# Kernel optimization log

Hardware: AMD Instinct MI355X
Metric: run time of the kernel (lower is better)

Reference implementation:

```python
import jax, jax.numpy as jnp
import numpy as np
from jax.scipy.special import i0

# torchkbnufft default configuration
N = 256          # image size per dim (im_size)
OSF = 2          # grid oversampling factor (default grid_size = 2*im_size)
G = N * OSF      # oversampled grid size = 512
W = 6            # kernel width (numpoints default)
ALPHA = 2.34 * W # Kaiser-Bessel shape parameter (kbwidth default 2.34)
M = 65536        # number of non-uniform k-space samples
B, C = 2, 8      # batch, coils


def _kb_ft(t):
    """Analytic Fourier transform of the KB kernel (for deapodization)."""
    s2 = ALPHA ** 2 - (jnp.pi * W * t) ** 2
    z = jnp.sqrt(jnp.abs(s2)) + 1e-12
    return jnp.where(s2 >= 0, jnp.sinh(z) / z, jnp.sin(z) / z)


def _kb(d):
    """Kaiser-Bessel interpolation kernel, d = distance in grid units."""
    u = 1.0 - (2.0 * d / W) ** 2
    return jnp.where(u > 0, i0(ALPHA * jnp.sqrt(jnp.maximum(u, 1e-12))), 0.0) / W


def setup_inputs() -> dict:
    key = jax.random.key(0)
    k1, k2 = jax.random.split(key)
    x_image = jax.random.normal(k1, (B, C, N, N), dtype=jnp.float32)
    # trajectory in radians/sample, uniform in [-pi, pi)
    k_traj = (jax.random.uniform(k2, (2, M), dtype=jnp.float32) - 0.5) * (2 * jnp.pi)
    return {"x_image": x_image, "k_traj": k_traj}


def reference(x_image, k_traj):
    # 1) deapodization (scaling coefficients), centered image convention
    n = jnp.arange(N, dtype=jnp.float32) - N / 2
    sc = 1.0 / _kb_ft(n / G)                       # (N,)
    xs = (x_image * (sc[:, None] * sc[None, :])).astype(jnp.complex64)

    # 2) zero-pad onto oversampled grid with image centered at index 0 (mod G)
    grid = jnp.zeros(x_image.shape[:2] + (G, G), jnp.complex64)
    grid = grid.at[..., :N, :N].set(xs)
    grid = jnp.roll(grid, shift=(-(N // 2), -(N // 2)), axis=(-2, -1))
    Xk = jnp.fft.fft2(grid)                        # (B,C,G,G) uniform k-space

    # 3) KB interpolation onto non-uniform points (irregular gather)
    tm = k_traj * (G / (2 * jnp.pi))               # continuous grid coords, (2,M)
    offs = jnp.arange(-(W // 2) + 1, W // 2 + 1, dtype=jnp.float32)  # [-2..3]
    base = jnp.floor(tm)
    pts = base[:, :, None] + offs                  # (2,M,W) neighbor coords
    wts = _kb(tm[:, :, None] - pts)                # (2,M,W) real weights
    idx = pts.astype(jnp.int32) % G                # wrap (periodic grid)

    gathered = Xk[:, :, idx[0][:, :, None], idx[1][:, None, :]]  # (B,C,M,W,W)
    y = jnp.einsum('bcmij,mi,mj->bcm', gathered,
                   wts[0].astype(jnp.complex64), wts[1].astype(jnp.complex64))
    # return complex result as stacked (real, imag) float32 for the harness
    return jnp.stack([y.real, y.imag], axis=-1)   # (B,C,M,2)
```

## Files before the change

kernel.cpp:

```cpp
#include <hip/hip_runtime.h>
#include <hip/hip_fp16.h>
#include <math.h>

#define NN 256
#define GSZ 512
#define GG (GSZ * GSZ)
#define BC 16
#define MM 65536
#define ALPHA_C 14.04f
#define WKER 6
#define PI_F 3.14159265358979f
#define RC2 0.70710678118654752f
#define KSCALE 81.48733086305042f

#define SSCALE 16777216.0f
#define INV_SSCALE 5.9604644775390625e-8f

#define CAP 144
#define TRW 21
#define TPITCH 23
#define PLANE (TRW * TPITCH)
#define QPL 4
#define NPQ (QPL * TRW * TRW)

__device__ __forceinline__ __half2* gh_plane(float2* grid, int bc) {
    return (__half2*)((char*)grid + (size_t)bc * (GG * 8) + 524288);
}
__device__ __forceinline__ const __half2* gh_plane_c(const float2* grid, int bc) {
    return (const __half2*)((const char*)grid + (size_t)bc * (GG * 8) + 524288);
}


__device__ __forceinline__ float bessel_i0(float x) {
    if (x < 3.75f) {
        float t = x * (1.0f / 3.75f);
        float t2 = t * t;
        return 1.0f + t2 * (3.5156229f + t2 * (3.0899424f + t2 * (1.2067492f +
                     t2 * (0.2659732f + t2 * (0.0360768f + t2 * 0.0045813f)))));
    } else {
        float t = 3.75f / x;
        float p = 0.39894228f + t * (0.01328592f + t * (0.00225319f + t * (-0.00157565f +
                  t * (0.00916281f + t * (-0.02057706f + t * (0.02635537f +
                  t * (-0.01647633f + t * 0.00392377f)))))));
        return p * __expf(x) * rsqrtf(x);
    }
}

__device__ __forceinline__ float kb_weight(float d) {
    float r = d * (2.0f / (float)WKER);
    float u = 1.0f - r * r;
    if (u <= 0.0f) return 0.0f;
    return bessel_i0(ALPHA_C * sqrtf(u)) * (1.0f / (float)WKER);
}

__device__ __forceinline__ float kb_ft_inv(float t) {
    float a = PI_F * (float)WKER * t;
    float s2 = ALPHA_C * ALPHA_C - a * a;
    float z = sqrtf(fabsf(s2)) + 1e-12f;
    float sh = 0.5f * (__expf(z) - __expf(-z));
    return z / sh;
}

__device__ __forceinline__ void cmul(float& zr, float& zi, float wr, float wi) {
    float r = zr * wr - zi * wi;
    zi = zr * wi + zi * wr;
    zr = r;
}


template <int L>
__device__ __forceinline__ void radix8_stage(float* pr, float* pi_, int j) {
    int pos = j & (L - 1);
    int base = (j - pos) * 8 + pos;
    float ar[8], ai[8];
#pragma unroll
    for (int r = 0; r < 8; ++r) {
        int idx = base + r * L;
        int ph = idx + (idx >> 3);
        ar[r] = pr[ph];
        ai[r] = pi_[ph];
    }
    if (L > 1) {
        float th = (float)pos * (-PI_F / (4.0f * (float)L));
        float s1, c1;
        __sincosf(th, &s1, &c1);
        float wr = c1, wi = s1;
#pragma unroll
        for (int r = 1; r < 8; ++r) {
            cmul(ar[r], ai[r], wr, wi);
            float nr = wr * c1 - wi * s1;
            wi = wr * s1 + wi * c1;
            wr = nr;
        }
    }
    float s0r = ar[0] + ar[4], s0i = ai[0] + ai[4];
    float d0r = ar[0] - ar[4], d0i = ai[0] - ai[4];
    float s1r = ar[2] + ar[6], s1i = ai[2] + ai[6];
    float d1r = ar[2] - ar[6], d1i = ai[2] - ai[6];
    float E0r = s0r + s1r, E0i = s0i + s1i;
    float E2r = s0r - s1r, E2i = s0i - s1i;
    float E1r = d0r + d1i, E1i = d0i - d1r;
    float E3r = d0r - d1i, E3i = d0i + d1r;
    float u0r = ar[1] + ar[5], u0i = ai[1] + ai[5];
    float v0r = ar[1] - ar[5], v0i = ai[1] - ai[5];
    float u1r = ar[3] + ar[7], u1i = ai[3] + ai[7];
    float v1r = ar[3] - ar[7], v1i = ai[3] - ai[7];
    float O0r = u0r + u1r, O0i = u0i + u1i;
    float O2r = u0r - u1r, O2i = u0i - u1i;
    float O1r = v0r + v1i, O1i = v0i - v1r;
    float O3r = v0r - v1i, O3i = v0i + v1r;
    float t1r = RC2 * (O1r + O1i), t1i = RC2 * (O1i - O1r);
    float t2r = O2i,               t2i = -O2r;
    float t3r = RC2 * (O3i - O3r), t3i = -RC2 * (O3r + O3i);
    float xr[8], xi[8];
    xr[0] = E0r + O0r; xi[0] = E0i + O0i;
    xr[4] = E0r - O0r; xi[4] = E0i - O0i;
    xr[1] = E1r + t1r; xi[1] = E1i + t1i;
    xr[5] = E1r - t1r; xi[5] = E1i - t1i;
    xr[2] = E2r + t2r; xi[2] = E2i + t2i;
    xr[6] = E2r - t2r; xi[6] = E2i - t2i;
    xr[3] = E3r + t3r; xi[3] = E3i + t3i;
    xr[7] = E3r - t3r; xi[7] = E3i - t3i;
#pragma unroll
    for (int q = 0; q < 8; ++q) {
        int idx = base + q * L;
        int ph = idx + (idx >> 3);
        pr[ph] = xr[q];
        pi_[ph] = xi[q];
    }
}


#define LDSP 576
#define ROWBLK (BC * 64)
__global__ void __launch_bounds__(256) k_fft_row_bin(
    const float* __restrict__ x, float2* __restrict__ grid,
    const float* __restrict__ kt, unsigned* __restrict__ cnt,
    unsigned* __restrict__ meta, __half2* __restrict__ whalf) {
    __shared__ float re[4][LDSP], im[4][LDSP];
    int b = blockIdx.x;
    int t = threadIdx.x;
    if (b >= ROWBLK) {
        int m = (b - ROWBLK) * 256 + t;
        float tmx = kt[m] * KSCALE;
        float tmy = kt[MM + m] * KSCALE;
        float bx = floorf(tmx), by = floorf(tmy);
        int ibx = (int)bx & (GSZ - 1);
        int iby = (int)by & (GSZ - 1);
        int tile = ((ibx >> 4) << 5) | (iby >> 4);
        unsigned slot = atomicAdd(&cnt[tile], 1u);
        if (slot < CAP) {
            int idx = tile * CAP + (int)slot;
            int lx = ibx & 15;
            int ly = iby & 15;
            meta[idx] = ((unsigned)m << 8) | (unsigned)(lx << 4) | (unsigned)ly;
            float w0[6], w1[6];
#pragma unroll
            for (int o = 0; o < 6; ++o) {
                float offv = (float)(o - 2);
                w0[o] = kb_weight(tmx - (bx + offv));
                w1[o] = kb_weight(tmy - (by + offv));
            }
            __half2* wp = whalf + (size_t)idx * 6;
            wp[0] = __half2(__float2half_rn(w0[0]), __float2half_rn(w0[1]));
            wp[1] = __half2(__float2half_rn(w0[2]), __float2half_rn(w0[3]));
            wp[2] = __half2(__float2half_rn(w0[4]), __float2half_rn(w0[5]));
            wp[3] = __half2(__float2half_rn(w1[0]), __float2half_rn(w1[1]));
            wp[4] = __half2(__float2half_rn(w1[2]), __float2half_rn(w1[3]));
            wp[5] = __half2(__float2half_rn(w1[4]), __float2half_rn(w1[5]));
        }
        return;
    }
    int w = t >> 6;
    int l = t & 63;
    int rg = (b & 63) * 4 + w;
    int bc = b >> 6;
    int r = (rg < 128) ? rg : rg + 256;
    int r_img = rg ^ 128;
    float scx = kb_ft_inv((float)(r_img - 128) * (1.0f / (float)GSZ));
    const float* xrow = x + ((size_t)bc * NN + (size_t)r_img) * NN;
#pragma unroll
    for (int e = 0; e < 8; ++e) {
        int i = e * 64 + l;
        float v = 0.0f;
        if (i < 128 || i >= 384) {
            int y = (i + 128) & (GSZ - 1);
            float scy = kb_ft_inv((float)(y - 128) * (1.0f / (float)GSZ));
            v = xrow[y] * scx * scy;
        }
        int rev = (l & 7) * 64 + (l >> 3) * 8 + e;
        int ph = rev + (rev >> 3);
        re[w][ph] = v;
        im[w][ph] = 0.0f;
    }
    __syncthreads();
    radix8_stage<1>(re[w], im[w], l);
    __syncthreads();
    radix8_stage<8>(re[w], im[w], l);
    __syncthreads();
    radix8_stage<64>(re[w], im[w], l);
    __syncthreads();
    size_t gbase = (size_t)bc * GG + (size_t)r * GSZ;
#pragma unroll
    for (int e = 0; e < 8; ++e) {
        int k = e * 64 + l;
        int ph = k + (k >> 3);
        grid[gbase + k] = make_float2(re[w][ph], im[w][ph]);
    }
}


#define CSTR 577
__global__ void __launch_bounds__(256) k_fft_col(float2* __restrict__ grid) {
    __shared__ float re[16][CSTR], im[16][CSTR];
    int b = blockIdx.x;
    int bc = b >> 5;
    int c0 = (b & 31) << 4;
    size_t base = (size_t)bc * GG + (size_t)c0;
    int t = threadIdx.x;
#pragma unroll
    for (int it = 0; it < 32; ++it) {
        int idx = it * 256 + t;
        int row = idx >> 4, col = idx & 15;
        float2 v = make_float2(0.0f, 0.0f);
        if (row < 128 || row >= 384)
            v = grid[base + (size_t)row * GSZ + col];
        int rev = (row & 7) * 64 + ((row >> 3) & 7) * 8 + (row >> 6);
        int ph = rev + (rev >> 3);
        re[col][ph] = v.x;
        im[col][ph] = v.y;
    }
    __syncthreads();
    int col = t & 15, jg = t >> 4;
#pragma unroll
    for (int k = 0; k < 4; ++k) radix8_stage<1>(re[col], im[col], jg + 16 * k);
    __syncthreads();
#pragma unroll
    for (int k = 0; k < 4; ++k) radix8_stage<8>(re[col], im[col], jg + 16 * k);
    __syncthreads();
#pragma unroll
    for (int k = 0; k < 4; ++k) radix8_stage<64>(re[col], im[col], jg + 16 * k);
    __syncthreads();
    __half2* ghp = gh_plane(grid, bc);
#pragma unroll
    for (int it = 0; it < 32; ++it) {
        int idx = it * 256 + t;
        int row = idx >> 4, c = idx & 15;
        int ph = row + (row >> 3);
        ghp[(size_t)row * GSZ + c0 + c] = __float22half2_rn(
            make_float2(re[c][ph] * SSCALE, im[c][ph] * SSCALE));
    }
}


__global__ void __launch_bounds__(128, 6) k_gather_tile(
    const float2* __restrict__ grid, const unsigned* __restrict__ cnt,
    const unsigned* __restrict__ meta, const __half2* __restrict__ whalf,
    float2* __restrict__ out) {
    __shared__ __half2 ldsh[QPL * PLANE];
    int bid = blockIdx.x;
    int b = ((bid & 7) << 9) | (bid >> 3);
    int tile = b >> 2;
    int quad = b & 3;
    int bc0 = quad * QPL;
    int tx0 = (tile >> 5) << 4;
    int ty0 = (tile & 31) << 4;
    int t = threadIdx.x;
#pragma unroll
    for (int k = 0; k < 14; ++k) {
        int idx = t + (k << 7);
        if (idx < NPQ) {
            int p = idx / (TRW * TRW);
            int rem = idx - p * (TRW * TRW);
            int r = rem / TRW;
            int c = rem - r * TRW;
            int row = (tx0 - 2 + r) & (GSZ - 1);
            int col = (ty0 - 2 + c) & (GSZ - 1);
            ldsh[p * PLANE + r * TPITCH + c] =
                gh_plane_c(grid, bc0 + p)[(size_t)row * GSZ + col];
        }
    }
    int n = (int)cnt[tile];
    if (n > CAP) n = CAP;
    __syncthreads();
    int g = t >> 6;
    int baseA = (2 * g) * PLANE;
    int baseB = baseA + PLANE;
    int bcA = bc0 + 2 * g, bcB = bcA + 1;
    for (int s = (t & 63); s < n; s += 64) {
        int idx = tile * CAP + s;
        unsigned mc = meta[idx];
        int m = (int)(mc >> 8);
        int lx = (int)((mc >> 4) & 15u);
        int ly = (int)(mc & 15u);
        const __half2* wp = whalf + (size_t)idx * 6;
        __half2 p0 = wp[0], p1 = wp[1], p2 = wp[2];
        __half2 q0 = wp[3], q1 = wp[4], q2 = wp[5];
        float w0v[6], w1v[6];
        w0v[0] = __low2float(p0) * INV_SSCALE;
        w0v[1] = __high2float(p0) * INV_SSCALE;
        w0v[2] = __low2float(p1) * INV_SSCALE;
        w0v[3] = __high2float(p1) * INV_SSCALE;
        w0v[4] = __low2float(p2) * INV_SSCALE;
        w0v[5] = __high2float(p2) * INV_SSCALE;
        w1v[0] = __low2float(q0);
        w1v[1] = __high2float(q0);
        w1v[2] = __low2float(q1);
        w1v[3] = __high2float(q1);
        w1v[4] = __low2float(q2);
        w1v[5] = __high2float(q2);
        int off0 = lx * TPITCH + ly;
        float arA = 0.f, aiA = 0.f, arB = 0.f, aiB = 0.f;
#pragma unroll
        for (int ii = 0; ii < 6; ++ii) {
            float wi = w0v[ii];
            int rowoff = off0 + ii * TPITCH;
#pragma unroll
            for (int j = 0; j < 6; ++j) {
                float wv = wi * w1v[j];
                int o = rowoff + j;
                float2 vA = __half22float2(ldsh[baseA + o]);
                float2 vB = __half22float2(ldsh[baseB + o]);
                arA = fmaf(wv, vA.x, arA);
                aiA = fmaf(wv, vA.y, aiA);
                arB = fmaf(wv, vB.x, arB);
                aiB = fmaf(wv, vB.y, aiB);
            }
        }
        out[(size_t)bcA * MM + m] = make_float2(arA, aiA);
        out[(size_t)bcB * MM + m] = make_float2(arB, aiB);
    }
}

__global__ void k_gather(const float2* __restrict__ grid, const float* __restrict__ kt,
                         float2* __restrict__ out) {
    int tid = blockIdx.x * blockDim.x + threadIdx.x;
    int m = tid & (MM - 1);
    int bc = tid >> 16;
    float tmx = kt[m] * KSCALE;
    float tmy = kt[MM + m] * KSCALE;
    float bx = floorf(tmx), by = floorf(tmy);
    int ibx = (int)bx, iby = (int)by;
    float w0[6], w1[6];
    int ix[6], iy[6];
#pragma unroll
    for (int o = 0; o < 6; ++o) {
        float offv = (float)(o - 2);
        w0[o] = kb_weight(tmx - (bx + offv)) * INV_SSCALE;
        w1[o] = kb_weight(tmy - (by + offv));
        ix[o] = (ibx + (o - 2) + GSZ) & (GSZ - 1);
        iy[o] = (iby + (o - 2) + GSZ) & (GSZ - 1);
    }
    const __half2* img = gh_plane_c(grid, bc);
    float ar = 0.0f, ai = 0.0f;
#pragma unroll
    for (int i = 0; i < 6; ++i) {
        const __half2* rowp = img + (size_t)ix[i] * GSZ;
        float wi = w0[i];
#pragma unroll
        for (int j = 0; j < 6; ++j) {
            float2 v = __half22float2(rowp[iy[j]]);
            float wv = wi * w1[j];
            ar = fmaf(wv, v.x, ar);
            ai = fmaf(wv, v.y, ai);
        }
    }
    out[(size_t)bc * MM + m] = make_float2(ar, ai);
}

__global__ void __launch_bounds__(256) k_fft_row(const float* __restrict__ x,
                                                 float2* __restrict__ grid) {
    __shared__ float re[4][LDSP], im[4][LDSP];
    int b = blockIdx.x;
    int t = threadIdx.x;
    int w = t >> 6;
    int l = t & 63;
    int rg = (b & 63) * 4 + w;
    int bc = b >> 6;
    int r = (rg < 128) ? rg : rg + 256;
    int r_img = rg ^ 128;
    float scx = kb_ft_inv((float)(r_img - 128) * (1.0f / (float)GSZ));
    const float* xrow = x + ((size_t)bc * NN + (size_t)r_img) * NN;
#pragma unroll
    for (int e = 0; e < 8; ++e) {
        int i = e * 64 + l;
        float v = 0.0f;
        if (i < 128 || i >= 384) {
            int y = (i + 128) & (GSZ - 1);
            float scy = kb_ft_inv((float)(y - 128) * (1.0f / (float)GSZ));
            v = xrow[y] * scx * scy;
        }
        int rev = (l & 7) * 64 + (l >> 3) * 8 + e;
        int ph = rev + (rev >> 3);
        re[w][ph] = v;
        im[w][ph] = 0.0f;
    }
    __syncthreads();
    radix8_stage<1>(re[w], im[w], l);
    __syncthreads();
    radix8_stage<8>(re[w], im[w], l);
    __syncthreads();
    radix8_stage<64>(re[w], im[w], l);
    __syncthreads();
    size_t gbase = (size_t)bc * GG + (size_t)r * GSZ;
#pragma unroll
    for (int e = 0; e < 8; ++e) {
        int k = e * 64 + l;
        int ph = k + (k >> 3);
        grid[gbase + k] = make_float2(re[w][ph], im[w][ph]);
    }
}


extern "C" void kernel_launch(void* const* d_in, const int* in_sizes, int n_in,
                              void* d_out, int out_size, void* d_ws, size_t ws_size,
                              hipStream_t stream) {
    const float* x = (const float*)d_in[0];
    const float* kt = (const float*)d_in[1];
    float2* out = (float2*)d_out;
    char* ws = (char*)d_ws;

    const size_t GRID_BYTES = (size_t)BC * GG * sizeof(float2);
    const size_t CNT_BYTES = 1024 * sizeof(unsigned);
    const size_t META_BYTES = (size_t)1024 * CAP * sizeof(unsigned);
    const size_t WH_BYTES = (size_t)1024 * CAP * 6 * sizeof(__half2);
    float2* grid = (float2*)ws;
    unsigned* cnt = (unsigned*)(ws + GRID_BYTES);
    unsigned* meta = (unsigned*)(ws + GRID_BYTES + CNT_BYTES);
    __half2* whalf = (__half2*)(ws + GRID_BYTES + CNT_BYTES + META_BYTES);
    const size_t NEED = GRID_BYTES + CNT_BYTES + META_BYTES + WH_BYTES;

    if (ws_size >= NEED) {
        hipMemsetAsync(cnt, 0, CNT_BYTES, stream);
        k_fft_row_bin<<<ROWBLK + 256, 256, 0, stream>>>(x, grid, kt, cnt, meta, whalf);
        k_fft_col<<<BC * (GSZ / 16), 256, 0, stream>>>(grid);
        k_gather_tile<<<4096, 128, 0, stream>>>(grid, cnt, meta, whalf, out);
    } else {
        k_fft_row<<<BC * 64, 256, 0, stream>>>(x, grid);
        k_fft_col<<<BC * (GSZ / 16), 256, 0, stream>>>(grid);
        k_gather<<<(BC * MM) / 256, 256, 0, stream>>>(grid, kt, out);
    }
}
```

Before: 67.65 us.

## Gather 8 coil planes per tile block and widen column FFT blocks to 512 threads

```diff
diff --git a/kernel.cpp b/kernel.cpp
--- a/kernel.cpp
+++ b/kernel.cpp
@@ -20,7 +20,7 @@
 #define TRW 21
 #define TPITCH 23
 #define PLANE (TRW * TPITCH)
-#define QPL 4
+#define QPL 8
 #define NPQ (QPL * TRW * TRW)
 
 __device__ __forceinline__ __half2* gh_plane(float2* grid, int bc) {
@@ -211,7 +211,7 @@
 
 
 #define CSTR 577
-__global__ void __launch_bounds__(256) k_fft_col(float2* __restrict__ grid) {
+__global__ void __launch_bounds__(512) k_fft_col(float2* __restrict__ grid) {
     __shared__ float re[16][CSTR], im[16][CSTR];
     int b = blockIdx.x;
     int bc = b >> 5;
@@ -219,8 +219,8 @@
     size_t base = (size_t)bc * GG + (size_t)c0;
     int t = threadIdx.x;
 #pragma unroll
-    for (int it = 0; it < 32; ++it) {
-        int idx = it * 256 + t;
+    for (int it = 0; it < 16; ++it) {
+        int idx = it * 512 + t;
         int row = idx >> 4, col = idx & 15;
         float2 v = make_float2(0.0f, 0.0f);
         if (row < 128 || row >= 384)
@@ -233,18 +233,18 @@
     __syncthreads();
     int col = t & 15, jg = t >> 4;
 #pragma unroll
-    for (int k = 0; k < 4; ++k) radix8_stage<1>(re[col], im[col], jg + 16 * k);
-    __syncthreads();
-#pragma unroll
-    for (int k = 0; k < 4; ++k) radix8_stage<8>(re[col], im[col], jg + 16 * k);
-    __syncthreads();
-#pragma unroll
-    for (int k = 0; k < 4; ++k) radix8_stage<64>(re[col], im[col], jg + 16 * k);
+    for (int k = 0; k < 2; ++k) radix8_stage<1>(re[col], im[col], jg + 32 * k);
+    __syncthreads();
+#pragma unroll
+    for (int k = 0; k < 2; ++k) radix8_stage<8>(re[col], im[col], jg + 32 * k);
+    __syncthreads();
+#pragma unroll
+    for (int k = 0; k < 2; ++k) radix8_stage<64>(re[col], im[col], jg + 32 * k);
     __syncthreads();
     __half2* ghp = gh_plane(grid, bc);
 #pragma unroll
-    for (int it = 0; it < 32; ++it) {
-        int idx = it * 256 + t;
+    for (int it = 0; it < 16; ++it) {
+        int idx = it * 512 + t;
         int row = idx >> 4, c = idx & 15;
         int ph = row + (row >> 3);
         ghp[(size_t)row * GSZ + c0 + c] = __float22half2_rn(
@@ -259,15 +259,15 @@
     float2* __restrict__ out) {
     __shared__ __half2 ldsh[QPL * PLANE];
     int bid = blockIdx.x;
-    int b = ((bid & 7) << 9) | (bid >> 3);
-    int tile = b >> 2;
-    int quad = b & 3;
-    int bc0 = quad * QPL;
+    int b = ((bid & 7) << 8) | (bid >> 3);
+    int tile = b >> 1;
+    int oct = b & 1;
+    int bc0 = oct * QPL;
     int tx0 = (tile >> 5) << 4;
     int ty0 = (tile & 31) << 4;
     int t = threadIdx.x;
 #pragma unroll
-    for (int k = 0; k < 14; ++k) {
+    for (int k = 0; k < 28; ++k) {
         int idx = t + (k << 7);
         if (idx < NPQ) {
             int p = idx / (TRW * TRW);
@@ -284,9 +284,11 @@
     if (n > CAP) n = CAP;
     __syncthreads();
     int g = t >> 6;
-    int baseA = (2 * g) * PLANE;
-    int baseB = baseA + PLANE;
-    int bcA = bc0 + 2 * g, bcB = bcA + 1;
+    int base0 = (4 * g) * PLANE;
+    int base1 = base0 + PLANE;
+    int base2 = base1 + PLANE;
+    int base3 = base2 + PLANE;
+    int bcw = bc0 + 4 * g;
     for (int s = (t & 63); s < n; s += 64) {
         int idx = tile * CAP + s;
         unsigned mc = meta[idx];
@@ -310,7 +312,8 @@
         w1v[4] = __low2float(q2);
         w1v[5] = __high2float(q2);
         int off0 = lx * TPITCH + ly;
-        float arA = 0.f, aiA = 0.f, arB = 0.f, aiB = 0.f;
+        float ar0 = 0.f, ai0 = 0.f, ar1 = 0.f, ai1 = 0.f;
+        float ar2 = 0.f, ai2 = 0.f, ar3 = 0.f, ai3 = 0.f;
 #pragma unroll
         for (int ii = 0; ii < 6; ++ii) {
             float wi = w0v[ii];
@@ -319,16 +322,24 @@
             for (int j = 0; j < 6; ++j) {
                 float wv = wi * w1v[j];
                 int o = rowoff + j;
-                float2 vA = __half22float2(ldsh[baseA + o]);
-                float2 vB = __half22float2(ldsh[baseB + o]);
-                arA = fmaf(wv, vA.x, arA);
-                aiA = fmaf(wv, vA.y, aiA);
-                arB = fmaf(wv, vB.x, arB);
-                aiB = fmaf(wv, vB.y, aiB);
+                float2 v0 = __half22float2(ldsh[base0 + o]);
+                float2 v1 = __half22float2(ldsh[base1 + o]);
+                float2 v2 = __half22float2(ldsh[base2 + o]);
+                float2 v3 = __half22float2(ldsh[base3 + o]);
+                ar0 = fmaf(wv, v0.x, ar0);
+                ai0 = fmaf(wv, v0.y, ai0);
+                ar1 = fmaf(wv, v1.x, ar1);
+                ai1 = fmaf(wv, v1.y, ai1);
+                ar2 = fmaf(wv, v2.x, ar2);
+                ai2 = fmaf(wv, v2.y, ai2);
+                ar3 = fmaf(wv, v3.x, ar3);
+                ai3 = fmaf(wv, v3.y, ai3);
             }
         }
-        out[(size_t)bcA * MM + m] = make_float2(arA, aiA);
-        out[(size_t)bcB * MM + m] = make_float2(arB, aiB);
+        out[(size_t)(bcw + 0) * MM + m] = make_float2(ar0, ai0);
+        out[(size_t)(bcw + 1) * MM + m] = make_float2(ar1, ai1);
+        out[(size_t)(bcw + 2) * MM + m] = make_float2(ar2, ai2);
+        out[(size_t)(bcw + 3) * MM + m] = make_float2(ar3, ai3);
     }
 }
 
@@ -433,11 +444,11 @@
     if (ws_size >= NEED) {
         hipMemsetAsync(cnt, 0, CNT_BYTES, stream);
         k_fft_row_bin<<<ROWBLK + 256, 256, 0, stream>>>(x, grid, kt, cnt, meta, whalf);
-        k_fft_col<<<BC * (GSZ / 16), 256, 0, stream>>>(grid);
-        k_gather_tile<<<4096, 128, 0, stream>>>(grid, cnt, meta, whalf, out);
+        k_fft_col<<<BC * (GSZ / 16), 512, 0, stream>>>(grid);
+        k_gather_tile<<<2048, 128, 0, stream>>>(grid, cnt, meta, whalf, out);
     } else {
         k_fft_row<<<BC * 64, 256, 0, stream>>>(x, grid);
-        k_fft_col<<<BC * (GSZ / 16), 256, 0, stream>>>(grid);
+        k_fft_col<<<BC * (GSZ / 16), 512, 0, stream>>>(grid);
         k_gather<<<(BC * MM) / 256, 256, 0, stream>>>(grid, kt, out);
     }
 }
```

New measurement: 67.51 us. About the same (-0.2%).
